# Kernel optimization log

Measured on AMD Instinct MI355X. Metric: run time of the kernel, lower is better.

## Reference

```python
import jax, jax.numpy as jnp
import numpy as np

H = 64          # nheads
NH = 8          # lru_dim // nheads (per-head state dim, must be even)
LRU_DIM = 512
HIDDEN = 512
BATCH = 8
T = 4096
MAX_PHASE = 6.28
R_MIN, R_MAX = 0.9, 0.999


def setup_inputs() -> dict:
    key = jax.random.key(0)
    ks = jax.random.split(key, 8)
    input_sequence = jax.random.normal(ks[0], (BATCH, 1, HIDDEN, 1, T), dtype=jnp.float32)
    # theta_init: log(uniform(0, max_phase)), shape (lru_dim//2, 1)
    theta_log = jnp.log(jax.random.uniform(ks[1], (LRU_DIM // 2, 1), maxval=MAX_PHASE))
    # ortho_mat_init(lru_dim, N)
    P = jax.random.normal(ks[2], (LRU_DIM, NH)) / jnp.sqrt(NH + LRU_DIM)
    # mat_init(lru_dim, hidden_dim)
    B = jax.random.normal(ks[3], (LRU_DIM, HIDDEN)) / jnp.sqrt(HIDDEN + LRU_DIM)
    # mat_init(hidden_dim, lru_dim)
    C = jax.random.normal(ks[4], (HIDDEN, LRU_DIM)) / jnp.sqrt(HIDDEN + LRU_DIM)
    D = jax.random.normal(ks[5], (HIDDEN,))
    # nu_log_init: log(-log r) interpolated by uniform
    u1 = jax.random.uniform(ks[6], (H,))
    gamma_log = jnp.log(-jnp.log(R_MAX)) + u1 * (jnp.log(-jnp.log(R_MIN)) - jnp.log(-jnp.log(R_MAX)))
    return dict(input_sequence=input_sequence, theta_log=theta_log, P=P, B=B, C=C, D=D,
                gamma_log=gamma_log)


def _mix_sequence(gamma, thetas, Us):
    """Single head. gamma: scalar, thetas: (N/2,), Us: (T, B, N) -> (T, B, N)."""
    def binf(a, b):
        g_i, th_i, acc_i = a
        g_j, th_j, acc_j = b
        # rotate-half (RoPE-style) of accumulated state
        rot = jnp.stack([-acc_i[..., 1::2], acc_i[..., 0::2]], axis=-1).reshape(acc_i.shape)
        theta = jnp.repeat(th_j[..., None], 2, axis=-1).reshape(th_j.shape[:-1] + (th_j.shape[-1] * 2,))
        sin = jnp.sin(theta)[..., None, :]  # (..., 1, N)
        cos = jnp.cos(theta)[..., None, :]
        acc = g_j[..., None, None] * (cos * acc_i + sin * rot)
        return (g_i * g_j, th_i + th_j, acc + acc_j)

    Tlen = Us.shape[0]
    gammas = jnp.repeat(gamma[None], Tlen, axis=0)          # (T,)
    Rs = jnp.repeat(thetas[None, :], Tlen, axis=0)          # (T, N/2)
    _, _, res = jax.lax.associative_scan(binf, (gammas, Rs, Us))
    return res


def reference(input_sequence, theta_log, P, B, C, D, gamma_log):
    x = input_sequence[:, 0, :, 0].transpose(0, 2, 1)       # (B, T, hidden)
    bsz, Tlen, _ = x.shape
    thetas = jnp.exp(theta_log.reshape(H, NH // 2))          # (H, N/2)
    Pm = P.reshape(H, NH, NH)
    Bm = B.reshape(H, NH, HIDDEN)
    gamma = jnp.exp(-jnp.exp(gamma_log))                     # (H,)
    # trace(B B^T) per head == sum of squares
    trace_per_head = jnp.sum(Bm * Bm, axis=(1, 2))
    norm = jnp.sqrt((1.0 - gamma ** 2) / trace_per_head)
    B_norm = norm[:, None, None] * Bm                        # (H, N, hidden)
    # orthogonalize P via matrix exponential of skew-symmetric part
    Pm = jax.vmap(jax.scipy.linalg.expm)(Pm - Pm.transpose(0, 2, 1))  # (H, N, N)
    Us = jnp.einsum('HnD,BTD->HTBn', B_norm, x)              # project inputs per head
    Us = jnp.einsum('HnN,HTBn->HTBN', Pm.transpose(0, 2, 1), Us)
    y = jax.vmap(_mix_sequence)(gamma, thetas, Us)           # (H, T, B, N)
    y = jnp.einsum('HNn,HTBN->HTBn', Pm, y)
    y = y.transpose(2, 1, 0, 3).reshape(bsz, Tlen, -1)       # (B, T, lru_dim)
    y = jnp.einsum('Dn,BTn->BTD', C, y) + D * x
    return y[0]                                              # (T, hidden)
```

## Files before the change

### kernel.cpp

```cpp
#include <hip/hip_runtime.h>
#include <math.h>

#define NHEADS   64
#define TLEN     4096
#define CHUNK    16
#define NCHUNK   256

typedef unsigned short u16;
typedef unsigned int   u32;
typedef __attribute__((ext_vector_type(8))) short bf16x8;
typedef __attribute__((ext_vector_type(4))) float f32x4;

__device__ __forceinline__ u16 f2bf(float x) {
    u32 u = __float_as_uint(x);
    u32 r = (u + 0x7FFFu + ((u >> 16) & 1u)) >> 16;
    return (u16)r;
}
__device__ __forceinline__ float bf2f(u16 h) { return __uint_as_float(((u32)h) << 16); }


__global__ void k_setup(const float* __restrict__ P,
                        const float* __restrict__ Bmat,
                        const float* __restrict__ theta_log,
                        const float* __restrict__ gamma_log,
                        float* __restrict__ ws) {
    __shared__ double As[8][8];
    __shared__ double Rs[8][8];
    __shared__ double red[64];
    __shared__ int sh_s;
    const int h = blockIdx.x;
    const int tid = threadIdx.x;
    const int i = tid >> 3, j = tid & 7;

    As[i][j] = (double)P[(h*8 + i)*8 + j] - (double)P[(h*8 + j)*8 + i];

    const float* Bh = Bmat + h*8*512;
    double ss = 0.0;
    for (int q = 0; q < 64; ++q) { float v = Bh[q*64 + tid]; ss += (double)v * (double)v; }
    red[tid] = ss;
    __syncthreads();

    if (tid == 0) {
        double nrm = 0.0;
        for (int r = 0; r < 8; ++r) {
            double rs = 0.0;
            for (int c = 0; c < 8; ++c) rs += fabs(As[r][c]);
            nrm = fmax(nrm, rs);
        }
        int s = 0;
        while (nrm > 0.25 && s < 40) { nrm *= 0.5; ++s; }
        sh_s = s;
        double tr = 0.0;
        for (int q = 0; q < 64; ++q) tr += red[q];
        double ed = exp((double)gamma_log[h]);
        double g  = exp(-ed);
        ws[4096 + h] = (float)g;
        ws[4416 + h] = (float)sqrt((1.0 - g*g) / tr);
    }
    if (tid < 4) ws[4160 + h*4 + tid] = expf(theta_log[h*4 + tid]);
    __syncthreads();

    const double sc = ldexp(1.0, -sh_s);
    As[i][j] *= sc;
    const int NT = 13;
    Rs[i][j] = (i == j ? 1.0 : 0.0) + As[i][j] / (double)NT;
    __syncthreads();
    for (int k = NT - 1; k >= 1; --k) {
        double t = 0.0;
        #pragma unroll
        for (int m = 0; m < 8; ++m) t += As[i][m] * Rs[m][j];
        __syncthreads();
        Rs[i][j] = (i == j ? 1.0 : 0.0) + t / (double)k;
        __syncthreads();
    }
    for (int q = 0; q < sh_s; ++q) {
        double t = 0.0;
        #pragma unroll
        for (int m = 0; m < 8; ++m) t += Rs[i][m] * Rs[m][j];
        __syncthreads();
        Rs[i][j] = t;
        __syncthreads();
    }
    ws[h*64 + i*8 + j] = (float)Rs[i][j];
}

__global__ void k_proj(const float* __restrict__ Bmat,
                       const float* __restrict__ C,
                       const float* __restrict__ ws_ro,
                       u16* __restrict__ W1pk,
                       u16* __restrict__ CEpk) {
    const int gid = blockIdx.x * 256 + threadIdx.x;
    if (gid < 512*512) {
        const int k = gid >> 9, d = gid & 511;
        const int h = k >> 3, N = k & 7;
        const float* Pm = ws_ro + h*64 + N*8;
        const float nrm = ws_ro[4416 + h];
        float acc = 0.f;
        #pragma unroll
        for (int n = 0; n < 8; ++n) acc += Pm[n] * Bmat[(h*8 + n)*512 + d];
        acc *= nrm;
        u16 hi = f2bf(acc), lo = f2bf(acc - bf2f(hi));
        W1pk[k*1024 + d] = hi;
        W1pk[k*1024 + 512 + d] = lo;
    } else {
        const int g2 = gid - 512*512;
        const int e = g2 >> 9, k = g2 & 511;
        const int h = k >> 3, N = k & 7;
        const float* Pm = ws_ro + h*64 + N*8;
        float acc = 0.f;
        #pragma unroll
        for (int n = 0; n < 8; ++n) acc += Pm[n] * C[e*512 + h*8 + n];
        u16 hi = f2bf(acc), lo = f2bf(acc - bf2f(hi));
        CEpk[e*1024 + k] = hi;
        CEpk[e*1024 + 512 + k] = lo;
    }
}

__global__ void k_xt(const float* __restrict__ X, u16* __restrict__ XT) {
    __shared__ float Xs[64][65];
    const int tid = threadIdx.x;
    const int t0 = blockIdx.x * 64, d0 = blockIdx.y * 64;
    {
        const int dr = tid >> 4, tc = (tid & 15) * 4;
        #pragma unroll
        for (int it = 0; it < 4; ++it) {
            const int dd = it*16 + dr;
            float4 v = *reinterpret_cast<const float4*>(X + (size_t)(d0 + dd)*4096 + t0 + tc);
            Xs[dd][tc] = v.x; Xs[dd][tc+1] = v.y; Xs[dd][tc+2] = v.z; Xs[dd][tc+3] = v.w;
        }
    }
    __syncthreads();
    const int tr = tid >> 2, ds = (tid & 3) * 16;
    u32 hb[8], lb[8];
    #pragma unroll
    for (int j = 0; j < 16; j += 2) {
        float a = Xs[ds + j][tr], b = Xs[ds + j + 1][tr];
        u16 ha = f2bf(a), la = f2bf(a - bf2f(ha));
        u16 hbb = f2bf(b), lbb = f2bf(b - bf2f(hbb));
        hb[j >> 1] = (u32)ha | ((u32)hbb << 16);
        lb[j >> 1] = (u32)la | ((u32)lbb << 16);
    }
    u16* orow = XT + (size_t)(t0 + tr)*1024 + d0 + ds;
    uint4 h0; h0.x = hb[0]; h0.y = hb[1]; h0.z = hb[2]; h0.w = hb[3];
    uint4 h1; h1.x = hb[4]; h1.y = hb[5]; h1.z = hb[6]; h1.w = hb[7];
    uint4 l0; l0.x = lb[0]; l0.y = lb[1]; l0.z = lb[2]; l0.w = lb[3];
    uint4 l1; l1.x = lb[4]; l1.y = lb[5]; l1.z = lb[6]; l1.w = lb[7];
    *reinterpret_cast<uint4*>(orow)       = h0;
    *reinterpret_cast<uint4*>(orow + 8)   = h1;
    *reinterpret_cast<uint4*>(orow + 512) = l0;
    *reinterpret_cast<uint4*>(orow + 520) = l1;
}

#define MFMA_BF16(A_, B_, C_) __builtin_amdgcn_mfma_f32_16x16x32_bf16(A_, B_, C_, 0, 0, 0)
template<int EPI>
__global__ __launch_bounds__(256) void k_gemm(const u16* __restrict__ Apk,
                                              const u16* __restrict__ Bpk,
                                              float* __restrict__ Cout,
                                              const u16* __restrict__ XT,
                                              const float* __restrict__ Dvec) {
    __shared__ u16 Ah[64*72], Al[64*72], Bh[64*72], Bl[64*72];
    const int tid = threadIdx.x;
    const int bid = blockIdx.x;
    const int tile = (bid & 7) * 64 + (bid >> 3);
    const int mt = tile >> 3, nt = tile & 7;
    const int m0 = mt * 64, n0 = nt * 64;
    const int lane = tid & 63, wid = tid >> 6;
    const int wm = wid >> 1, wn = wid & 1;
    const int lr = lane & 15, lc = lane >> 4;
    const int sr = tid >> 2, ss = (tid & 3) * 16;

    f32x4 acc00 = {0.f,0.f,0.f,0.f}, acc01 = acc00, acc10 = acc00, acc11 = acc00;

    const u16* Arow = Apk + (size_t)(m0 + sr)*1024 + ss;
    const u16* Brow = Bpk + (size_t)(n0 + sr)*1024 + ss;

    for (int k0 = 0; k0 < 512; k0 += 64) {
        float4 vah0 = *reinterpret_cast<const float4*>(Arow + k0);
        float4 vah1 = *reinterpret_cast<const float4*>(Arow + k0 + 8);
        float4 val0 = *reinterpret_cast<const float4*>(Arow + 512 + k0);
        float4 val1 = *reinterpret_cast<const float4*>(Arow + 512 + k0 + 8);
        float4 vbh0 = *reinterpret_cast<const float4*>(Brow + k0);
        float4 vbh1 = *reinterpret_cast<const float4*>(Brow + k0 + 8);
        float4 vbl0 = *reinterpret_cast<const float4*>(Brow + 512 + k0);
        float4 vbl1 = *reinterpret_cast<const float4*>(Brow + 512 + k0 + 8);
        *reinterpret_cast<float4*>(&Ah[sr*72 + ss])     = vah0;
        *reinterpret_cast<float4*>(&Ah[sr*72 + ss + 8]) = vah1;
        *reinterpret_cast<float4*>(&Al[sr*72 + ss])     = val0;
        *reinterpret_cast<float4*>(&Al[sr*72 + ss + 8]) = val1;
        *reinterpret_cast<float4*>(&Bh[sr*72 + ss])     = vbh0;
        *reinterpret_cast<float4*>(&Bh[sr*72 + ss + 8]) = vbh1;
        *reinterpret_cast<float4*>(&Bl[sr*72 + ss])     = vbl0;
        *reinterpret_cast<float4*>(&Bl[sr*72 + ss + 8]) = vbl1;
        __syncthreads();
        #pragma unroll
        for (int kk = 0; kk < 2; ++kk) {
            const int ko = kk*32 + lc*8;
            const int ra0 = (wm*32 + lr)*72 + ko,  ra1 = ra0 + 16*72;
            const int rb0 = (wn*32 + lr)*72 + ko,  rb1 = rb0 + 16*72;
            bf16x8 fah0 = *reinterpret_cast<const bf16x8*>(&Ah[ra0]);
            bf16x8 fah1 = *reinterpret_cast<const bf16x8*>(&Ah[ra1]);
            bf16x8 fal0 = *reinterpret_cast<const bf16x8*>(&Al[ra0]);
            bf16x8 fal1 = *reinterpret_cast<const bf16x8*>(&Al[ra1]);
            bf16x8 fbh0 = *reinterpret_cast<const bf16x8*>(&Bh[rb0]);
            bf16x8 fbh1 = *reinterpret_cast<const bf16x8*>(&Bh[rb1]);
            bf16x8 fbl0 = *reinterpret_cast<const bf16x8*>(&Bl[rb0]);
            bf16x8 fbl1 = *reinterpret_cast<const bf16x8*>(&Bl[rb1]);
            acc00 = MFMA_BF16(fah0, fbl0, acc00);
            acc00 = MFMA_BF16(fal0, fbh0, acc00);
            acc00 = MFMA_BF16(fah0, fbh0, acc00);
            acc01 = MFMA_BF16(fah0, fbl1, acc01);
            acc01 = MFMA_BF16(fal0, fbh1, acc01);
            acc01 = MFMA_BF16(fah0, fbh1, acc01);
            acc10 = MFMA_BF16(fah1, fbl0, acc10);
            acc10 = MFMA_BF16(fal1, fbh0, acc10);
            acc10 = MFMA_BF16(fah1, fbh0, acc10);
            acc11 = MFMA_BF16(fah1, fbl1, acc11);
            acc11 = MFMA_BF16(fal1, fbh1, acc11);
            acc11 = MFMA_BF16(fah1, fbh1, acc11);
        }
        __syncthreads();
    }

    #pragma unroll
    for (int im = 0; im < 2; ++im) {
        #pragma unroll
        for (int in = 0; in < 2; ++in) {
            f32x4 v = (im == 0) ? (in == 0 ? acc00 : acc01)
                                : (in == 0 ? acc10 : acc11);
            const int row0 = m0 + wm*32 + im*16 + lc*4;
            const int col  = n0 + wn*32 + in*16 + lr;
            if (EPI == 0) {
                #pragma unroll
                for (int rg = 0; rg < 4; ++rg)
                    Cout[(size_t)(row0 + rg)*512 + col] = v[rg];
            } else {
                const float dv = Dvec[col];
                #pragma unroll
                for (int rg = 0; rg < 4; ++rg) {
                    const int t = row0 + rg;
                    float xv = bf2f(XT[(size_t)t*1024 + col]) + bf2f(XT[(size_t)t*1024 + 512 + col]);
                    Cout[(size_t)t*512 + col] = v[rg] + dv*xv;
                }
            }
        }
    }
}

__global__ void k_scan(float* __restrict__ U, float* __restrict__ E,
                       const float* __restrict__ ws_ro) {
    const int c = blockIdx.x;
    const int p = threadIdx.x;
    const float th = ws_ro[4160 + p];
    const float g  = ws_ro[4096 + (p >> 2)];
    const float cs = cosf(th), sn = sinf(th);
    float* base = U + (size_t)c*CHUNK*512 + 2*p;
    float2 u[CHUNK];
    #pragma unroll
    for (int i = 0; i < CHUNK; ++i) u[i] = *reinterpret_cast<float2*>(base + (size_t)i*512);
    float h0 = 0.f, h1 = 0.f;
    #pragma unroll
    for (int i = 0; i < CHUNK; ++i) {
        float n0 = g*(cs*h0 - sn*h1) + u[i].x;
        float n1 = g*(sn*h0 + cs*h1) + u[i].y;
        h0 = n0; h1 = n1;
        u[i] = make_float2(n0, n1);
    }
    #pragma unroll
    for (int i = 0; i < CHUNK; ++i) *reinterpret_cast<float2*>(base + (size_t)i*512) = u[i];
    E[c*512 + 2*p]     = h0;
    E[c*512 + 2*p + 1] = h1;
}

__global__ void k_carry(const float* __restrict__ E, float* __restrict__ S,
                        float* __restrict__ TAB,
                        const float* __restrict__ theta_log,
                        const float* __restrict__ gamma_log) {
    const int p = threadIdx.x;
    const double th = exp((double)theta_log[p]);
    const double ed = exp((double)gamma_log[p >> 2]);
    const double g  = exp(-ed);
    const double cd = cos(th), sd = sin(th);
    double gc = g*cd, gs = g*sd;
    for (int i = 0; i < CHUNK; ++i) {
        if (i) {
            double t0 = g*(cd*gc - sd*gs);
            double t1 = g*(sd*gc + cd*gs);
            gc = t0; gs = t1;
        }
        TAB[(i*256 + p)*2 + 0] = (float)gc;
        TAB[(i*256 + p)*2 + 1] = (float)gs;
    }
    const float fLc = (float)gc, fLs = (float)gs;
    float s0 = 0.f, s1 = 0.f;
    S[2*p] = 0.f; S[2*p + 1] = 0.f;
    const float* Ep = E + 2*p;
    float* Sp = S + 2*p;
    float2 bA[16], bB[16];
    #pragma unroll
    for (int j = 0; j < 16; ++j) bA[j] = *reinterpret_cast<const float2*>(Ep + (size_t)j*512);
    for (int bb = 0; bb < 8; ++bb) {
        const int b0 = 2*bb, b1 = 2*bb + 1;
        #pragma unroll
        for (int j = 0; j < 16; ++j)
            bB[j] = *reinterpret_cast<const float2*>(Ep + (size_t)(b1*16 + j)*512);
        #pragma unroll
        for (int j = 0; j < 16; ++j) {
            const int c = b0*16 + j + 1;
            float n0 = fLc*s0 - fLs*s1 + bA[j].x;
            float n1 = fLs*s0 + fLc*s1 + bA[j].y;
            s0 = n0; s1 = n1;
            *reinterpret_cast<float2*>(Sp + (size_t)c*512) = make_float2(s0, s1);
        }
        if (b1 + 1 < 16) {
            #pragma unroll
            for (int j = 0; j < 16; ++j)
                bA[j] = *reinterpret_cast<const float2*>(Ep + (size_t)((b1 + 1)*16 + j)*512);
        }
        #pragma unroll
        for (int j = 0; j < 16; ++j) {
            const int c = b1*16 + j + 1;
            float n0 = fLc*s0 - fLs*s1 + bB[j].x;
            float n1 = fLs*s0 + fLc*s1 + bB[j].y;
            s0 = n0; s1 = n1;
            if (c < NCHUNK)
                *reinterpret_cast<float2*>(Sp + (size_t)c*512) = make_float2(s0, s1);
        }
    }
}

__global__ void k_fixpack(float* __restrict__ U, const float* __restrict__ S,
                          const float* __restrict__ TAB) {
    const int t = blockIdx.x*4 + (threadIdx.x >> 6);
    const int l = threadIdx.x & 63;
    float* row = U + (size_t)t*512;
    float4 v0 = *reinterpret_cast<float4*>(row + l*4);
    float4 v1 = *reinterpret_cast<float4*>(row + 256 + l*4);
    const int c = t >> 4, i = t & 15;
    float4 tb0 = *reinterpret_cast<const float4*>(TAB + ((size_t)i*256 + 2*l)*2);
    float4 sv0 = *reinterpret_cast<const float4*>(S + (size_t)c*512 + 4*l);
    float4 tb1 = *reinterpret_cast<const float4*>(TAB + ((size_t)i*256 + 128 + 2*l)*2);
    float4 sv1 = *reinterpret_cast<const float4*>(S + (size_t)c*512 + 256 + 4*l);
    v0.x += tb0.x*sv0.x - tb0.y*sv0.y;  v0.y += tb0.y*sv0.x + tb0.x*sv0.y;
    v0.z += tb0.z*sv0.z - tb0.w*sv0.w;  v0.w += tb0.w*sv0.z + tb0.z*sv0.w;
    v1.x += tb1.x*sv1.x - tb1.y*sv1.y;  v1.y += tb1.y*sv1.x + tb1.x*sv1.y;
    v1.z += tb1.z*sv1.z - tb1.w*sv1.w;  v1.w += tb1.w*sv1.z + tb1.z*sv1.w;
    u16 h0x = f2bf(v0.x), h0y = f2bf(v0.y), h0z = f2bf(v0.z), h0w = f2bf(v0.w);
    u16 h1x = f2bf(v1.x), h1y = f2bf(v1.y), h1z = f2bf(v1.z), h1w = f2bf(v1.w);
    u16 l0x = f2bf(v0.x - bf2f(h0x)), l0y = f2bf(v0.y - bf2f(h0y));
    u16 l0z = f2bf(v0.z - bf2f(h0z)), l0w = f2bf(v0.w - bf2f(h0w));
    u16 l1x = f2bf(v1.x - bf2f(h1x)), l1y = f2bf(v1.y - bf2f(h1y));
    u16 l1z = f2bf(v1.z - bf2f(h1z)), l1w = f2bf(v1.w - bf2f(h1w));
    u16* ur = reinterpret_cast<u16*>(row);
    uint2 w0; w0.x = (u32)h0x | ((u32)h0y << 16); w0.y = (u32)h0z | ((u32)h0w << 16);
    uint2 w1; w1.x = (u32)h1x | ((u32)h1y << 16); w1.y = (u32)h1z | ((u32)h1w << 16);
    uint2 w2; w2.x = (u32)l0x | ((u32)l0y << 16); w2.y = (u32)l0z | ((u32)l0w << 16);
    uint2 w3; w3.x = (u32)l1x | ((u32)l1y << 16); w3.y = (u32)l1z | ((u32)l1w << 16);
    *reinterpret_cast<uint2*>(ur + 4*l)       = w0;
    *reinterpret_cast<uint2*>(ur + 256 + 4*l) = w1;
    *reinterpret_cast<uint2*>(ur + 512 + 4*l) = w2;
    *reinterpret_cast<uint2*>(ur + 768 + 4*l) = w3;
}

extern "C" void kernel_launch(void* const* d_in, const int* in_sizes, int n_in,
                              void* d_out, int out_size, void* d_ws, size_t ws_size,
                              hipStream_t stream) {
    const float* X  = (const float*)d_in[0];
    const float* th = (const float*)d_in[1];
    const float* P  = (const float*)d_in[2];
    const float* Bm = (const float*)d_in[3];
    const float* C  = (const float*)d_in[4];
    const float* Dv = (const float*)d_in[5];
    const float* gl = (const float*)d_in[6];
    char* wsb = (char*)d_ws;
    float* ws   = (float*)wsb;
    u16*   W1pk = (u16*)(wsb + 32768);
    u16*   CEpk = (u16*)(wsb + 1081344);
    u16*   XTpk = (u16*)(wsb + 2129920);
    float* U    = (float*)(wsb + 10518528);
    float* E    = (float*)(wsb + 18907136);
    float* S    = (float*)(wsb + 19431424);
    float* TAB  = (float*)(wsb + 19955712);
    float* out  = (float*)d_out;

    k_setup<<<NHEADS, 64, 0, stream>>>(P, Bm, th, gl, ws);
    k_proj<<<2048, 256, 0, stream>>>(Bm, C, ws, W1pk, CEpk);
    k_xt<<<dim3(64, 8), 256, 0, stream>>>(X, XTpk);
    k_gemm<0><<<512, 256, 0, stream>>>(XTpk, W1pk, U, XTpk, Dv);
    k_scan<<<NCHUNK, 256, 0, stream>>>(U, E, ws);
    k_carry<<<1, 256, 0, stream>>>(E, S, TAB, th, gl);
    k_fixpack<<<1024, 256, 0, stream>>>(U, S, TAB);
    k_gemm<1><<<512, 256, 0, stream>>>((const u16*)U, CEpk, out, XTpk, Dv);
}
```

Before: 163.3 us.

## Fuse chunk scan into first GEMM epilogue and carry fix into second GEMM prologue

The intra-chunk recurrence now runs inside the first GEMM's epilogue on the tile staged in shared memory, and the inter-chunk carry correction plus bf16 hi/lo split now runs inside the second GEMM's A-operand load. This removes the separate k_scan and k_fixpack kernels, their launches, and extra global round trips of the U buffer. In exchange, only 128 of 256 threads do the serial scan in the epilogue, and the second GEMM reads fp32 U and applies the correction redundantly for each N-tile (8 times per row).

```diff
diff --git a/kernel.cpp b/kernel.cpp
--- a/kernel.cpp
+++ b/kernel.cpp
@@ -152,13 +152,24 @@
 }
 
 #define MFMA_BF16(A_, B_, C_) __builtin_amdgcn_mfma_f32_16x16x32_bf16(A_, B_, C_, 0, 0, 0)
-template<int EPI>
+template<int MODE>
 __global__ __launch_bounds__(256) void k_gemm(const u16* __restrict__ Apk,
+                                              const float* __restrict__ Af,
                                               const u16* __restrict__ Bpk,
                                               float* __restrict__ Cout,
                                               const u16* __restrict__ XT,
-                                              const float* __restrict__ Dvec) {
-    __shared__ u16 Ah[64*72], Al[64*72], Bh[64*72], Bl[64*72];
+                                              const float* __restrict__ Dvec,
+                                              const float* __restrict__ wsro,
+                                              float* __restrict__ E,
+                                              const float* __restrict__ S,
+                                              const float* __restrict__ TAB) {
+    __shared__ char smem[36864];
+    u16* Ah = (u16*)smem;
+    u16* Al = Ah + 4608;
+    u16* Bh = Al + 4608;
+    u16* Bl = Bh + 4608;
+    float* Ut = (float*)smem;
+
     const int tid = threadIdx.x;
     const int bid = blockIdx.x;
     const int tile = (bid & 7) * 64 + (bid >> 3);
@@ -171,22 +182,46 @@
 
     f32x4 acc00 = {0.f,0.f,0.f,0.f}, acc01 = acc00, acc10 = acc00, acc11 = acc00;
 
-    const u16* Arow = Apk + (size_t)(m0 + sr)*1024 + ss;
+    const int tA = m0 + sr;
+    const int cA = tA >> 4, iA = tA & 15;
     const u16* Brow = Bpk + (size_t)(n0 + sr)*1024 + ss;
+    const u16* Arow = (MODE == 0) ? (Apk + (size_t)tA*1024 + ss) : (const u16*)0;
+    const float* Urow = (MODE == 1) ? (Af + (size_t)tA*512 + ss) : (const float*)0;
 
     for (int k0 = 0; k0 < 512; k0 += 64) {
-        float4 vah0 = *reinterpret_cast<const float4*>(Arow + k0);
-        float4 vah1 = *reinterpret_cast<const float4*>(Arow + k0 + 8);
-        float4 val0 = *reinterpret_cast<const float4*>(Arow + 512 + k0);
-        float4 val1 = *reinterpret_cast<const float4*>(Arow + 512 + k0 + 8);
         float4 vbh0 = *reinterpret_cast<const float4*>(Brow + k0);
         float4 vbh1 = *reinterpret_cast<const float4*>(Brow + k0 + 8);
         float4 vbl0 = *reinterpret_cast<const float4*>(Brow + 512 + k0);
         float4 vbl1 = *reinterpret_cast<const float4*>(Brow + 512 + k0 + 8);
-        *reinterpret_cast<float4*>(&Ah[sr*72 + ss])     = vah0;
-        *reinterpret_cast<float4*>(&Ah[sr*72 + ss + 8]) = vah1;
-        *reinterpret_cast<float4*>(&Al[sr*72 + ss])     = val0;
-        *reinterpret_cast<float4*>(&Al[sr*72 + ss + 8]) = val1;
+        if constexpr (MODE == 0) {
+            float4 vah0 = *reinterpret_cast<const float4*>(Arow + k0);
+            float4 vah1 = *reinterpret_cast<const float4*>(Arow + k0 + 8);
+            float4 val0 = *reinterpret_cast<const float4*>(Arow + 512 + k0);
+            float4 val1 = *reinterpret_cast<const float4*>(Arow + 512 + k0 + 8);
+            *reinterpret_cast<float4*>(&Ah[sr*72 + ss])     = vah0;
+            *reinterpret_cast<float4*>(&Ah[sr*72 + ss + 8]) = vah1;
+            *reinterpret_cast<float4*>(&Al[sr*72 + ss])     = val0;
+            *reinterpret_cast<float4*>(&Al[sr*72 + ss + 8]) = val1;
+        } else {
+            const int p0 = (k0 + ss) >> 1;
+            #pragma unroll
+            for (int j = 0; j < 4; ++j) {
+                float4 u = *reinterpret_cast<const float4*>(Urow + k0 + 4*j);
+                float4 tb = *reinterpret_cast<const float4*>(TAB + ((size_t)iA*256 + p0 + 2*j)*2);
+                float4 sv = *reinterpret_cast<const float4*>(S + (size_t)cA*512 + 2*p0 + 4*j);
+                u.x += tb.x*sv.x - tb.y*sv.y;
+                u.y += tb.y*sv.x + tb.x*sv.y;
+                u.z += tb.z*sv.z - tb.w*sv.w;
+                u.w += tb.w*sv.z + tb.z*sv.w;
+                u16 hx = f2bf(u.x), hy = f2bf(u.y), hz = f2bf(u.z), hw = f2bf(u.w);
+                u16 lx = f2bf(u.x - bf2f(hx)), ly = f2bf(u.y - bf2f(hy));
+                u16 lz = f2bf(u.z - bf2f(hz)), lw = f2bf(u.w - bf2f(hw));
+                uint2 wh; wh.x = (u32)hx | ((u32)hy << 16); wh.y = (u32)hz | ((u32)hw << 16);
+                uint2 wl; wl.x = (u32)lx | ((u32)ly << 16); wl.y = (u32)lz | ((u32)lw << 16);
+                *reinterpret_cast<uint2*>(&Ah[sr*72 + ss + 4*j]) = wh;
+                *reinterpret_cast<uint2*>(&Al[sr*72 + ss + 4*j]) = wl;
+            }
+        }
         *reinterpret_cast<float4*>(&Bh[sr*72 + ss])     = vbh0;
         *reinterpret_cast<float4*>(&Bh[sr*72 + ss + 8]) = vbh1;
         *reinterpret_cast<float4*>(&Bl[sr*72 + ss])     = vbl0;
@@ -221,19 +256,56 @@
         __syncthreads();
     }
 
-    #pragma unroll
-    for (int im = 0; im < 2; ++im) {
-        #pragma unroll
-        for (int in = 0; in < 2; ++in) {
-            f32x4 v = (im == 0) ? (in == 0 ? acc00 : acc01)
-                                : (in == 0 ? acc10 : acc11);
-            const int row0 = m0 + wm*32 + im*16 + lc*4;
-            const int col  = n0 + wn*32 + in*16 + lr;
-            if (EPI == 0) {
+    if constexpr (MODE == 0) {
+        #pragma unroll
+        for (int im = 0; im < 2; ++im) {
+            #pragma unroll
+            for (int in = 0; in < 2; ++in) {
+                f32x4 v = (im == 0) ? (in == 0 ? acc00 : acc01)
+                                    : (in == 0 ? acc10 : acc11);
+                const int row0 = wm*32 + im*16 + lc*4;
+                const int col  = wn*32 + in*16 + lr;
                 #pragma unroll
                 for (int rg = 0; rg < 4; ++rg)
-                    Cout[(size_t)(row0 + rg)*512 + col] = v[rg];
-            } else {
+                    Ut[(row0 + rg)*72 + col] = v[rg];
+            }
+        }
+        __syncthreads();
+        if (tid < 128) {
+            const int cc = tid >> 5, pp = tid & 31;
+            const int pg = nt*32 + pp;
+            const float th = wsro[4160 + pg];
+            const float g  = wsro[4096 + (pg >> 2)];
+            const float cs = cosf(th), sn = sinf(th);
+            float h0 = 0.f, h1 = 0.f;
+            float* col = Ut + (cc*16)*72 + 2*pp;
+            #pragma unroll
+            for (int i = 0; i < CHUNK; ++i) {
+                float a = col[i*72], b = col[i*72 + 1];
+                float n0v = g*(cs*h0 - sn*h1) + a;
+                float n1v = g*(sn*h0 + cs*h1) + b;
+                col[i*72] = n0v; col[i*72 + 1] = n1v;
+                h0 = n0v; h1 = n1v;
+            }
+            E[(size_t)(mt*4 + cc)*512 + 2*pg]     = h0;
+            E[(size_t)(mt*4 + cc)*512 + 2*pg + 1] = h1;
+        }
+        __syncthreads();
+        const int row = tid >> 2, cseg = (tid & 3) * 16;
+        #pragma unroll
+        for (int j = 0; j < 4; ++j) {
+            float4 v = *reinterpret_cast<const float4*>(&Ut[row*72 + cseg + 4*j]);
+            *reinterpret_cast<float4*>(Cout + (size_t)(m0 + row)*512 + n0 + cseg + 4*j) = v;
+        }
+    } else {
+        #pragma unroll
+        for (int im = 0; im < 2; ++im) {
+            #pragma unroll
+            for (int in = 0; in < 2; ++in) {
+                f32x4 v = (im == 0) ? (in == 0 ? acc00 : acc01)
+                                    : (in == 0 ? acc10 : acc11);
+                const int row0 = m0 + wm*32 + im*16 + lc*4;
+                const int col  = n0 + wn*32 + in*16 + lr;
                 const float dv = Dvec[col];
                 #pragma unroll
                 for (int rg = 0; rg < 4; ++rg) {
@@ -244,31 +316,6 @@
             }
         }
     }
-}
-
-__global__ void k_scan(float* __restrict__ U, float* __restrict__ E,
-                       const float* __restrict__ ws_ro) {
-    const int c = blockIdx.x;
-    const int p = threadIdx.x;
-    const float th = ws_ro[4160 + p];
-    const float g  = ws_ro[4096 + (p >> 2)];
-    const float cs = cosf(th), sn = sinf(th);
-    float* base = U + (size_t)c*CHUNK*512 + 2*p;
-    float2 u[CHUNK];
-    #pragma unroll
-    for (int i = 0; i < CHUNK; ++i) u[i] = *reinterpret_cast<float2*>(base + (size_t)i*512);
-    float h0 = 0.f, h1 = 0.f;
-    #pragma unroll
-    for (int i = 0; i < CHUNK; ++i) {
-        float n0 = g*(cs*h0 - sn*h1) + u[i].x;
-        float n1 = g*(sn*h0 + cs*h1) + u[i].y;
-        h0 = n0; h1 = n1;
-        u[i] = make_float2(n0, n1);
-    }
-    #pragma unroll
-    for (int i = 0; i < CHUNK; ++i) *reinterpret_cast<float2*>(base + (size_t)i*512) = u[i];
-    E[c*512 + 2*p]     = h0;
-    E[c*512 + 2*p + 1] = h1;
 }
 
 __global__ void k_carry(const float* __restrict__ E, float* __restrict__ S,
@@ -326,39 +373,6 @@
                 *reinterpret_cast<float2*>(Sp + (size_t)c*512) = make_float2(s0, s1);
         }
     }
-}
-
-__global__ void k_fixpack(float* __restrict__ U, const float* __restrict__ S,
-                          const float* __restrict__ TAB) {
-    const int t = blockIdx.x*4 + (threadIdx.x >> 6);
-    const int l = threadIdx.x & 63;
-    float* row = U + (size_t)t*512;
-    float4 v0 = *reinterpret_cast<float4*>(row + l*4);
-    float4 v1 = *reinterpret_cast<float4*>(row + 256 + l*4);
-    const int c = t >> 4, i = t & 15;
-    float4 tb0 = *reinterpret_cast<const float4*>(TAB + ((size_t)i*256 + 2*l)*2);
-    float4 sv0 = *reinterpret_cast<const float4*>(S + (size_t)c*512 + 4*l);
-    float4 tb1 = *reinterpret_cast<const float4*>(TAB + ((size_t)i*256 + 128 + 2*l)*2);
-    float4 sv1 = *reinterpret_cast<const float4*>(S + (size_t)c*512 + 256 + 4*l);
-    v0.x += tb0.x*sv0.x - tb0.y*sv0.y;  v0.y += tb0.y*sv0.x + tb0.x*sv0.y;
-    v0.z += tb0.z*sv0.z - tb0.w*sv0.w;  v0.w += tb0.w*sv0.z + tb0.z*sv0.w;
-    v1.x += tb1.x*sv1.x - tb1.y*sv1.y;  v1.y += tb1.y*sv1.x + tb1.x*sv1.y;
-    v1.z += tb1.z*sv1.z - tb1.w*sv1.w;  v1.w += tb1.w*sv1.z + tb1.z*sv1.w;
-    u16 h0x = f2bf(v0.x), h0y = f2bf(v0.y), h0z = f2bf(v0.z), h0w = f2bf(v0.w);
-    u16 h1x = f2bf(v1.x), h1y = f2bf(v1.y), h1z = f2bf(v1.z), h1w = f2bf(v1.w);
-    u16 l0x = f2bf(v0.x - bf2f(h0x)), l0y = f2bf(v0.y - bf2f(h0y));
-    u16 l0z = f2bf(v0.z - bf2f(h0z)), l0w = f2bf(v0.w - bf2f(h0w));
-    u16 l1x = f2bf(v1.x - bf2f(h1x)), l1y = f2bf(v1.y - bf2f(h1y));
-    u16 l1z = f2bf(v1.z - bf2f(h1z)), l1w = f2bf(v1.w - bf2f(h1w));
-    u16* ur = reinterpret_cast<u16*>(row);
-    uint2 w0; w0.x = (u32)h0x | ((u32)h0y << 16); w0.y = (u32)h0z | ((u32)h0w << 16);
-    uint2 w1; w1.x = (u32)h1x | ((u32)h1y << 16); w1.y = (u32)h1z | ((u32)h1w << 16);
-    uint2 w2; w2.x = (u32)l0x | ((u32)l0y << 16); w2.y = (u32)l0z | ((u32)l0w << 16);
-    uint2 w3; w3.x = (u32)l1x | ((u32)l1y << 16); w3.y = (u32)l1z | ((u32)l1w << 16);
-    *reinterpret_cast<uint2*>(ur + 4*l)       = w0;
-    *reinterpret_cast<uint2*>(ur + 256 + 4*l) = w1;
-    *reinterpret_cast<uint2*>(ur + 512 + 4*l) = w2;
-    *reinterpret_cast<uint2*>(ur + 768 + 4*l) = w3;
 }
 
 extern "C" void kernel_launch(void* const* d_in, const int* in_sizes, int n_in,
@@ -385,9 +399,7 @@
     k_setup<<<NHEADS, 64, 0, stream>>>(P, Bm, th, gl, ws);
     k_proj<<<2048, 256, 0, stream>>>(Bm, C, ws, W1pk, CEpk);
     k_xt<<<dim3(64, 8), 256, 0, stream>>>(X, XTpk);
-    k_gemm<0><<<512, 256, 0, stream>>>(XTpk, W1pk, U, XTpk, Dv);
-    k_scan<<<NCHUNK, 256, 0, stream>>>(U, E, ws);
+    k_gemm<0><<<512, 256, 0, stream>>>(XTpk, (const float*)0, W1pk, U, XTpk, Dv, ws, E, S, TAB);
     k_carry<<<1, 256, 0, stream>>>(E, S, TAB, th, gl);
-    k_fixpack<<<1024, 256, 0, stream>>>(U, S, TAB);
-    k_gemm<1><<<512, 256, 0, stream>>>((const u16*)U, CEpk, out, XTpk, Dv);
-}
+    k_gemm<1><<<512, 256, 0, stream>>>((const u16*)0, U, CEpk, out, XTpk, Dv, ws, E, S, TAB);
+}
```

Result: no change. 161.0 us (-1.4%).
